# Performance work log

Measured on AMD Instinct MI355X. Metric: run time of the kernel, lower is better.

The kernel has to match this reference:

```python
import jax, jax.numpy as jnp
import numpy as np

TOP_K = 2
EPS = 1e-9

def setup_inputs() -> dict:
    key = jax.random.key(0)
    ks = jax.random.split(key, 8)
    B, L, C, F = 64, 512, 3, 300          # batteries, cycles, channels, curve length
    d_model, d_llm, d_ff, E = 512, 4096, 2048, 8
    s = lambda k, sh: jax.random.normal(k, sh, jnp.float32) * 0.02
    return dict(
        cycle_curve_data=jax.random.normal(ks[0], (B, L, C, F), jnp.float32),
        cycle_numbers=jax.random.uniform(ks[1], (B, 1), jnp.float32),
        DKP_embeddings=jax.random.normal(ks[2], (B, d_llm), jnp.float32),
        gate_W1=s(ks[3], (d_llm + 1, d_ff)), gate_b1=jnp.zeros((d_ff,), jnp.float32),
        gate_W2=s(ks[4], (d_ff, E)), gate_b2=jnp.zeros((E,), jnp.float32),
        expert_W=s(ks[5], (E, C * F, d_model)), expert_b=jnp.zeros((E, d_model), jnp.float32),
        gen_W=s(ks[6], (C * F, d_model)), gen_b=jnp.zeros((d_model,), jnp.float32),
    )

def reference(cycle_curve_data, cycle_numbers, DKP_embeddings,
              gate_W1, gate_b1, gate_W2, gate_b2,
              expert_W, expert_b, gen_W, gen_b):
    B, L, C, F = cycle_curve_data.shape
    # router (PatternRouter_two): 2-layer MLP over [DKP embedding ; cycle number]
    g_in = jnp.concatenate([DKP_embeddings, cycle_numbers], axis=-1)   # [B, d_llm+1]
    h = jax.nn.gelu(g_in @ gate_W1 + gate_b1)
    logits = h @ gate_W2 + gate_b2                                     # [B, E]
    # top-k mask on raw logits (as in source), softmax, mask, renormalize
    _, idx = jax.lax.top_k(logits, TOP_K)
    mask = jnp.zeros(logits.shape, bool).at[jnp.arange(B)[:, None], idx].set(True)
    p = jax.nn.softmax(logits, axis=1)
    g = jnp.where(mask, p, 0.0)
    gates = g / (jnp.sum(g, axis=1, keepdims=True) + EPS)              # [B, E]
    # experts: flatten(start_dim=2) then Linear(3*F -> d_model); combine is linear
    # so fold gates into a per-battery weight: sum_e gates[b,e] * W_e
    x = cycle_curve_data.reshape(B, L, C * F)                          # [B, L, 3F]
    Wb = jnp.einsum('be,eid->bid', gates, expert_W)                    # [B, 3F, d]
    bb = gates @ expert_b                                              # [B, d]
    moe_out = jnp.einsum('bli,bid->bld', x, Wb) + bb[:, None, :]       # [B, L, d]
    general = x @ gen_W + gen_b                                        # [B, L, d]
    # source casts the combined MoE output to bf16 before adding
    return general + moe_out.astype(jnp.bfloat16)
```

## Files before the change

kernel.cpp:

```cpp
#include <hip/hip_runtime.h>
#include <hip/hip_bf16.h>
#include <stdint.h>

typedef __attribute__((ext_vector_type(8))) short short8;
typedef __attribute__((ext_vector_type(4))) short short4v;
typedef __attribute__((ext_vector_type(4))) float f32x4;

__device__ inline unsigned short f2bf(float f) {
    union { float f; uint32_t u; } v; v.f = f;
    uint32_t u = v.u;
    uint32_t r = (u + 0x7FFFu + ((u >> 16) & 1u)) >> 16;
    return (unsigned short)r;
}

__device__ inline short4v pk4(float4 a) {
    short4v r;
    r[0] = (short)f2bf(a.x); r[1] = (short)f2bf(a.y);
    r[2] = (short)f2bf(a.z); r[3] = (short)f2bf(a.w);
    return r;
}

__global__ __launch_bounds__(256) void router1(const float* __restrict__ DKP,
                                               const float* __restrict__ W1,
                                               float* __restrict__ part) {
    __shared__ float gin[16 * 256];
    const int t   = threadIdx.x;
    const int lin = blockIdx.x + 16 * blockIdx.y;
    const int jc  = lin & 7;
    const int bg  = (lin >> 3) & 3;
    const int ks  = lin >> 5;
    const int k0  = ks * 256;
    {
        const int b = t >> 4, q = t & 15;
        #pragma unroll
        for (int s = 0; s < 4; ++s)
            *(float4*)(gin + b * 256 + q * 16 + s * 4) =
                *(const float4*)(DKP + (size_t)(bg * 16 + b) * 4096 + k0 + q * 16 + s * 4);
    }
    __syncthreads();
    const int ja = jc * 256 + t;
    float accA[16];
    #pragma unroll
    for (int b = 0; b < 16; ++b) accA[b] = 0.f;
    float wcur[8], wnxt[8];
    #pragma unroll
    for (int i = 0; i < 8; ++i)
        wcur[i] = W1[(size_t)(k0 + i) * 2048 + ja];
    #pragma unroll 2
    for (int oct = 0; oct < 32; ++oct) {
        const int kk = oct * 8;
        if (oct < 31) {
            #pragma unroll
            for (int i = 0; i < 8; ++i)
                wnxt[i] = W1[(size_t)(k0 + kk + 8 + i) * 2048 + ja];
        }
        #pragma unroll
        for (int b = 0; b < 16; ++b) {
            float4 g0 = *(const float4*)(gin + b * 256 + kk);
            float4 g1 = *(const float4*)(gin + b * 256 + kk + 4);
            accA[b] += g0.x*wcur[0] + g0.y*wcur[1] + g0.z*wcur[2] + g0.w*wcur[3]
                     + g1.x*wcur[4] + g1.y*wcur[5] + g1.z*wcur[6] + g1.w*wcur[7];
        }
        #pragma unroll
        for (int i = 0; i < 8; ++i) wcur[i] = wnxt[i];
    }
    #pragma unroll 1
    for (int b = 0; b < 16; ++b)
        part[((size_t)(ks * 64 + bg * 16 + b)) * 2048 + ja] = accA[b];
}

__global__ __launch_bounds__(256) void router2p(const float* __restrict__ part,
                                                const float* __restrict__ cyc,
                                                const float* __restrict__ W1,
                                                const float* __restrict__ b1,
                                                const float* __restrict__ W2,
                                                float* __restrict__ plog) {
    __shared__ float red[256 * 8];
    const int b = blockIdx.x, jc = blockIdx.y;
    const int t = threadIdx.x;
    const int j = jc * 256 + t;
    float s = 0.f;
    #pragma unroll
    for (int tt = 0; tt < 16; ++tt)
        s += part[((size_t)tt * 64 + b) * 2048 + j];
    s += cyc[b] * W1[(size_t)4096 * 2048 + j] + b1[j];
    const float u  = s + 0.044715f * s * s * s;
    const float th = tanhf(0.7978845608028654f * u);
    const float hv = 0.5f * s * (1.0f + th);
    const float* w = W2 + (size_t)j * 8;
    #pragma unroll
    for (int e = 0; e < 8; ++e) red[t * 8 + e] = hv * w[e];
    __syncthreads();
    if (t < 8) {
        float acc = 0.f;
        for (int r = 0; r < 256; ++r) acc += red[r * 8 + t];
        plog[((size_t)b * 8 + jc) * 8 + t] = acc;
    }
}

__global__ __launch_bounds__(64) void router4(const float* __restrict__ plog,
                                              const float* __restrict__ b2,
                                              float4* __restrict__ gates) {
    const int b = threadIdx.x;
    float l[8];
    #pragma unroll
    for (int e = 0; e < 8; ++e) l[e] = b2[e];
    #pragma unroll
    for (int jc = 0; jc < 8; ++jc)
        #pragma unroll
        for (int e = 0; e < 8; ++e)
            l[e] += plog[((size_t)b * 8 + jc) * 8 + e];
    int e0 = 0;
    #pragma unroll
    for (int e = 1; e < 8; ++e) if (l[e] > l[e0]) e0 = e;
    int e1 = (e0 == 0) ? 1 : 0;
    #pragma unroll
    for (int e = 0; e < 8; ++e) if (e != e0 && l[e] > l[e1]) e1 = e;
    const float m = l[e0];
    float p[8], Z = 0.f;
    #pragma unroll
    for (int e = 0; e < 8; ++e) { p[e] = expf(l[e] - m); Z += p[e]; }
    const float pe0 = p[e0] / Z, pe1 = p[e1] / Z;
    const float s2 = pe0 + pe1 + 1e-9f;
    gates[b] = make_float4(__int_as_float(e0), __int_as_float(e1), pe0 / s2, pe1 / s2);
}

__global__ __launch_bounds__(256) void combine_w(const float* __restrict__ genW,
                                                 const float* __restrict__ expW,
                                                 const float4* __restrict__ gates,
                                                 unsigned short* __restrict__ wc) {
    __shared__ float T[9][32 * 36];
    __shared__ float4 gsh[64];
    const int t  = threadIdx.x;
    const int d0 = blockIdx.x * 32;
    const int i0 = blockIdx.y * 32;
    if (t < 64) gsh[t] = gates[t];
    {
        const int il = t >> 3, d4 = (t & 7) * 4;
        const int i = i0 + il;
        const bool valid = (i < 900);
        const size_t off = (size_t)i * 512 + d0 + d4;
        #pragma unroll
        for (int s = 0; s < 9; ++s) {
            const float* src = (s == 0) ? genW : (expW + (size_t)(s - 1) * 900 * 512);
            float4 v = valid ? *(const float4*)(src + off) : make_float4(0, 0, 0, 0);
            float* Td = &T[s][0];
            Td[(d4 + 0) * 36 + il] = v.x;
            Td[(d4 + 1) * 36 + il] = v.y;
            Td[(d4 + 2) * 36 + il] = v.z;
            Td[(d4 + 3) * 36 + il] = v.w;
        }
    }
    __syncthreads();
    const int bb = t >> 7;
    const int dl = (t >> 2) & 31;
    const int sg = t & 3;
    const int fo = dl * 36 + sg * 8;
    unsigned short* wrow = wc + (size_t)(d0 + dl) * 928 + i0 + sg * 8;
    #pragma unroll 2
    for (int bp = 0; bp < 32; ++bp) {
        const int b = bp * 2 + bb;
        const float4 gt = gsh[b];
        const int e0 = __float_as_int(gt.x), e1 = __float_as_int(gt.y);
        const float g0 = gt.z, g1 = gt.w;
        float4 Ga = *(const float4*)&T[0][fo],      Gb = *(const float4*)&T[0][fo + 4];
        float4 Xa = *(const float4*)&T[1 + e0][fo], Xb = *(const float4*)&T[1 + e0][fo + 4];
        float4 Ya = *(const float4*)&T[1 + e1][fo], Yb = *(const float4*)&T[1 + e1][fo + 4];
        short8 r;
        r[0] = (short)f2bf(Ga.x + g0 * Xa.x + g1 * Ya.x);
        r[1] = (short)f2bf(Ga.y + g0 * Xa.y + g1 * Ya.y);
        r[2] = (short)f2bf(Ga.z + g0 * Xa.z + g1 * Ya.z);
        r[3] = (short)f2bf(Ga.w + g0 * Xa.w + g1 * Ya.w);
        r[4] = (short)f2bf(Gb.x + g0 * Xb.x + g1 * Yb.x);
        r[5] = (short)f2bf(Gb.y + g0 * Xb.y + g1 * Yb.y);
        r[6] = (short)f2bf(Gb.z + g0 * Xb.z + g1 * Yb.z);
        r[7] = (short)f2bf(Gb.w + g0 * Xb.w + g1 * Yb.w);
        *(short8*)(wrow + (size_t)b * 512 * 928) = r;
    }
}

__global__ __launch_bounds__(512) void moe_gemm(const float* __restrict__ x,
                                                const unsigned short* __restrict__ wc,
                                                const float4* __restrict__ gates,
                                                const float* __restrict__ eb,
                                                const float* __restrict__ genb,
                                                float* __restrict__ out) {
    __shared__ unsigned short As[2][64 * 40];
    __shared__ unsigned short Bs[4][512 * 32];
    const int g  = blockIdx.x;
    const int b  = (g & 7) + 8 * (g >> 6);
    const int m0 = ((g >> 3) & 7) * 64;
    const int t = threadIdx.x, lane = t & 63, wid = t >> 6;
    const float4 gt = gates[b];
    const int e0 = __float_as_int(gt.x), e1 = __float_as_int(gt.y);
    const float g0 = gt.z, g1 = gt.w;
    const float* xb = x + (size_t)b * 512 * 900;
    const unsigned short* wcb = wc + (size_t)b * 512 * 928;
    f32x4 acc[4][4];
    #pragma unroll
    for (int mi = 0; mi < 4; ++mi)
        #pragma unroll
        for (int ni = 0; ni < 4; ++ni)
            acc[mi][ni] = (f32x4){0.f, 0.f, 0.f, 0.f};

    const int arow  = t >> 3;
    const int akoff = (t & 7) * 4;
    const float* xrow = xb + (size_t)(m0 + arow) * 900 + akoff;
    const int bseg = (lane & 3) ^ ((lane >> 3) & 3);
    const int burow = lane >> 2;

    const int wn = wid * 64;
    const int lm = lane & 15, lq = lane >> 4;

    auto loadA = [&](int kt) -> float4 {
        if (kt < 28) return *(const float4*)(xrow + kt * 32);
        const float* p = xrow + 896 - (akoff ? 32 : 0);
        float4 raw = *(const float4*)p;
        if (akoff) raw = make_float4(0.f, 0.f, 0.f, 0.f);
        return raw;
    };
    auto stageB = [&](int buf, int kt) {
        const int k0 = kt * 32;
        #pragma unroll
        for (int r = 0; r < 4; ++r) {
            const int chunk = wid * 4 + r;
            const int n = chunk * 16 + burow;
            const unsigned short* gsrc = wcb + (size_t)n * 928 + k0 + bseg * 8;
            unsigned short* ldst = &Bs[buf][chunk * 512];
            __builtin_amdgcn_global_load_lds(
                (const __attribute__((address_space(1))) unsigned int*)gsrc,
                (__attribute__((address_space(3))) unsigned int*)ldst, 16, 0, 0);
        }
    };
    auto packA = [&](int buf, float4 f) {
        *(short4v*)&As[buf][arow * 40 + akoff] = pk4(f);
    };
    auto compute = [&](int buf) {
        short8 af[4], bfr[4];
        #pragma unroll
        for (int mi = 0; mi < 4; ++mi)
            af[mi] = *(const short8*)&As[buf & 1][(mi * 16 + lm) * 40 + lq * 8];
        #pragma unroll
        for (int ni = 0; ni < 4; ++ni) {
            const int n = wn + ni * 16 + lm;
            const int slot = lq ^ ((lm >> 1) & 3);
            bfr[ni] = *(const short8*)&Bs[buf][n * 32 + slot * 8];
        }
        #pragma unroll
        for (int mi = 0; mi < 4; ++mi)
            #pragma unroll
            for (int ni = 0; ni < 4; ++ni)
                acc[mi][ni] = __builtin_amdgcn_mfma_f32_16x16x32_bf16(
                    af[mi], bfr[ni], acc[mi][ni], 0, 0, 0);
    };

#define BARN(n) asm volatile("s_waitcnt vmcnt(" #n ") lgkmcnt(0)\n\ts_barrier" ::: "memory")

    float4 a_next;
    {
        float4 a0 = loadA(0);
        stageB(0, 0);
        a_next = loadA(1);
        stageB(1, 1);
        stageB(2, 2);
        packA(0, a0);
        BARN(9);
    }
    #pragma unroll 1
    for (int q = 0; q < 6; ++q) {
        const int tb = q * 4;
        { float4 a2 = loadA(tb + 2); stageB(3, tb + 3); compute(0); packA(1, a_next); a_next = a2; BARN(9); }
        { float4 a2 = loadA(tb + 3); stageB(0, tb + 4); compute(1); packA(0, a_next); a_next = a2; BARN(9); }
        { float4 a2 = loadA(tb + 4); stageB(1, tb + 5); compute(2); packA(1, a_next); a_next = a2; BARN(9); }
        { float4 a2 = loadA(tb + 5); stageB(2, tb + 6); compute(3); packA(0, a_next); a_next = a2; BARN(9); }
    }
    { float4 a2 = loadA(26); stageB(3, 27); compute(0); packA(1, a_next); a_next = a2; BARN(9); }
    { float4 a2 = loadA(27); stageB(0, 28); compute(1); packA(0, a_next); a_next = a2; BARN(9); }
    { float4 a2 = loadA(28); compute(2); packA(1, a_next); a_next = a2; BARN(5); }
    { compute(3); packA(0, a_next); BARN(0); }
    compute(0);

#undef BARN

    #pragma unroll
    for (int ni = 0; ni < 4; ++ni) {
        const int col = wn + ni * 16 + lm;
        const float bias = genb[col] + g0 * eb[e0 * 512 + col] + g1 * eb[e1 * 512 + col];
        #pragma unroll
        for (int mi = 0; mi < 4; ++mi) {
            const int row = m0 + mi * 16 + lq * 4;
            #pragma unroll
            for (int r = 0; r < 4; ++r)
                out[((size_t)b * 512 + row + r) * 512 + col] = acc[mi][ni][r] + bias;
        }
    }
}

extern "C" void kernel_launch(void* const* d_in, const int* in_sizes, int n_in,
                              void* d_out, int out_size, void* d_ws, size_t ws_size,
                              hipStream_t stream) {
    const float* x    = (const float*)d_in[0];
    const float* cyc  = (const float*)d_in[1];
    const float* dkp  = (const float*)d_in[2];
    const float* gW1  = (const float*)d_in[3];
    const float* gb1  = (const float*)d_in[4];
    const float* gW2  = (const float*)d_in[5];
    const float* gb2  = (const float*)d_in[6];
    const float* eW   = (const float*)d_in[7];
    const float* eb   = (const float*)d_in[8];
    const float* genW = (const float*)d_in[9];
    const float* genb = (const float*)d_in[10];
    float* out = (float*)d_out;

    char* ws = (char*)d_ws;
    unsigned short* wcomb = (unsigned short*)ws;
    float* part  = (float*)ws;
    float4* gts  = (float4*)(ws + 60817408);
    float* plog  = (float*)(ws + 60817408 + 1024);

    router1<<<dim3(16, 32), 256, 0, stream>>>(dkp, gW1, part);
    router2p<<<dim3(64, 8), 256, 0, stream>>>(part, cyc, gW1, gb1, gW2, plog);
    router4<<<1, 64, 0, stream>>>(plog, gb2, gts);
    combine_w<<<dim3(16, 29), 256, 0, stream>>>(genW, eW, gts, wcomb);
    moe_gemm<<<512, 512, 0, stream>>>(x, wcomb, gts, eb, genb, out);
}
```

Measured before the change: 335.2 us.

## Retile router and MoE GEMM, use k-slab weight layout and 128-row tiles

```diff
diff --git a/kernel.cpp b/kernel.cpp
--- a/kernel.cpp
+++ b/kernel.cpp
@@ -13,60 +13,62 @@
     return (unsigned short)r;
 }
 
-__device__ inline short4v pk4(float4 a) {
-    short4v r;
+__device__ inline short8 pk8(float4 a, float4 b) {
+    short8 r;
     r[0] = (short)f2bf(a.x); r[1] = (short)f2bf(a.y);
     r[2] = (short)f2bf(a.z); r[3] = (short)f2bf(a.w);
+    r[4] = (short)f2bf(b.x); r[5] = (short)f2bf(b.y);
+    r[6] = (short)f2bf(b.z); r[7] = (short)f2bf(b.w);
     return r;
 }
 
 __global__ __launch_bounds__(256) void router1(const float* __restrict__ DKP,
                                                const float* __restrict__ W1,
                                                float* __restrict__ part) {
-    __shared__ float gin[16 * 256];
-    const int t   = threadIdx.x;
-    const int lin = blockIdx.x + 16 * blockIdx.y;
-    const int jc  = lin & 7;
-    const int bg  = (lin >> 3) & 3;
-    const int ks  = lin >> 5;
-    const int k0  = ks * 256;
+    __shared__ float gin[16 * 64];
+    const int t  = threadIdx.x;
+    const int g  = blockIdx.x;
+    const int jc = g & 1;
+    const int bg = (g >> 3) & 3;
+    const int ks = ((g >> 1) & 3) | ((g >> 5) << 2);
+    const int k0 = ks * 64;
     {
-        const int b = t >> 4, q = t & 15;
-        #pragma unroll
-        for (int s = 0; s < 4; ++s)
-            *(float4*)(gin + b * 256 + q * 16 + s * 4) =
-                *(const float4*)(DKP + (size_t)(bg * 16 + b) * 4096 + k0 + q * 16 + s * 4);
+        const int bl = t >> 4, q = t & 15;
+        *(float4*)(gin + bl * 64 + q * 4) =
+            *(const float4*)(DKP + (size_t)(bg * 16 + bl) * 4096 + k0 + q * 4);
     }
     __syncthreads();
-    const int ja = jc * 256 + t;
-    float accA[16];
-    #pragma unroll
-    for (int b = 0; b < 16; ++b) accA[b] = 0.f;
-    float wcur[8], wnxt[8];
+    const int ja = jc * 1024 + t * 4;
+    f32x4 acc[16];
+    #pragma unroll
+    for (int bl = 0; bl < 16; ++bl) acc[bl] = (f32x4){0.f, 0.f, 0.f, 0.f};
+    f32x4 wcur[8], wnxt[8];
     #pragma unroll
     for (int i = 0; i < 8; ++i)
-        wcur[i] = W1[(size_t)(k0 + i) * 2048 + ja];
-    #pragma unroll 2
-    for (int oct = 0; oct < 32; ++oct) {
+        wcur[i] = *(const f32x4*)(W1 + (size_t)(k0 + i) * 2048 + ja);
+    #pragma unroll 1
+    for (int oct = 0; oct < 8; ++oct) {
         const int kk = oct * 8;
-        if (oct < 31) {
+        if (oct < 7) {
             #pragma unroll
             for (int i = 0; i < 8; ++i)
-                wnxt[i] = W1[(size_t)(k0 + kk + 8 + i) * 2048 + ja];
-        }
-        #pragma unroll
-        for (int b = 0; b < 16; ++b) {
-            float4 g0 = *(const float4*)(gin + b * 256 + kk);
-            float4 g1 = *(const float4*)(gin + b * 256 + kk + 4);
-            accA[b] += g0.x*wcur[0] + g0.y*wcur[1] + g0.z*wcur[2] + g0.w*wcur[3]
-                     + g1.x*wcur[4] + g1.y*wcur[5] + g1.z*wcur[6] + g1.w*wcur[7];
+                wnxt[i] = *(const f32x4*)(W1 + (size_t)(k0 + kk + 8 + i) * 2048 + ja);
+        }
+        #pragma unroll
+        for (int bl = 0; bl < 16; ++bl) {
+            float4 g0 = *(const float4*)(gin + bl * 64 + kk);
+            float4 g1 = *(const float4*)(gin + bl * 64 + kk + 4);
+            f32x4 a = acc[bl];
+            a = a + wcur[0] * g0.x + wcur[1] * g0.y + wcur[2] * g0.z + wcur[3] * g0.w
+                  + wcur[4] * g1.x + wcur[5] * g1.y + wcur[6] * g1.z + wcur[7] * g1.w;
+            acc[bl] = a;
         }
         #pragma unroll
         for (int i = 0; i < 8; ++i) wcur[i] = wnxt[i];
     }
     #pragma unroll 1
-    for (int b = 0; b < 16; ++b)
-        part[((size_t)(ks * 64 + bg * 16 + b)) * 2048 + ja] = accA[b];
+    for (int bl = 0; bl < 16; ++bl)
+        *(f32x4*)(part + ((size_t)(ks * 64 + bg * 16 + bl)) * 2048 + ja) = acc[bl];
 }
 
 __global__ __launch_bounds__(256) void router2p(const float* __restrict__ part,
@@ -80,8 +82,8 @@
     const int t = threadIdx.x;
     const int j = jc * 256 + t;
     float s = 0.f;
-    #pragma unroll
-    for (int tt = 0; tt < 16; ++tt)
+    #pragma unroll 8
+    for (int tt = 0; tt < 64; ++tt)
         s += part[((size_t)tt * 64 + b) * 2048 + j];
     s += cyc[b] * W1[(size_t)4096 * 2048 + j] + b1[j];
     const float u  = s + 0.044715f * s * s * s;
@@ -133,7 +135,8 @@
     __shared__ float4 gsh[64];
     const int t  = threadIdx.x;
     const int d0 = blockIdx.x * 32;
-    const int i0 = blockIdx.y * 32;
+    const int kt = blockIdx.y;
+    const int i0 = kt * 32;
     if (t < 64) gsh[t] = gates[t];
     {
         const int il = t >> 3, d4 = (t & 7) * 4;
@@ -156,7 +159,7 @@
     const int dl = (t >> 2) & 31;
     const int sg = t & 3;
     const int fo = dl * 36 + sg * 8;
-    unsigned short* wrow = wc + (size_t)(d0 + dl) * 928 + i0 + sg * 8;
+    unsigned short* wrow = wc + (size_t)kt * 16384 + (d0 + dl) * 32 + sg * 8;
     #pragma unroll 2
     for (int bp = 0; bp < 32; ++bp) {
         const int b = bp * 2 + bb;
@@ -175,120 +178,121 @@
         r[5] = (short)f2bf(Gb.y + g0 * Xb.y + g1 * Yb.y);
         r[6] = (short)f2bf(Gb.z + g0 * Xb.z + g1 * Yb.z);
         r[7] = (short)f2bf(Gb.w + g0 * Xb.w + g1 * Yb.w);
-        *(short8*)(wrow + (size_t)b * 512 * 928) = r;
-    }
-}
-
-__global__ __launch_bounds__(512) void moe_gemm(const float* __restrict__ x,
-                                                const unsigned short* __restrict__ wc,
-                                                const float4* __restrict__ gates,
-                                                const float* __restrict__ eb,
-                                                const float* __restrict__ genb,
-                                                float* __restrict__ out) {
-    __shared__ unsigned short As[2][64 * 40];
-    __shared__ unsigned short Bs[4][512 * 32];
+        *(short8*)(wrow + (size_t)b * 475136) = r;
+    }
+}
+
+__global__ __launch_bounds__(512, 1) void moe_gemm(const float* __restrict__ x,
+                                                   const unsigned short* __restrict__ wc,
+                                                   const float4* __restrict__ gates,
+                                                   const float* __restrict__ eb,
+                                                   const float* __restrict__ genb,
+                                                   float* __restrict__ out) {
+    __shared__ unsigned short As[2][128 * 40];
+    __shared__ unsigned short Bs[2][512 * 32];
     const int g  = blockIdx.x;
-    const int b  = (g & 7) + 8 * (g >> 6);
-    const int m0 = ((g >> 3) & 7) * 64;
+    const int b  = (g & 7) + 8 * (g >> 5);
+    const int m0 = ((g >> 3) & 3) * 128;
     const int t = threadIdx.x, lane = t & 63, wid = t >> 6;
     const float4 gt = gates[b];
     const int e0 = __float_as_int(gt.x), e1 = __float_as_int(gt.y);
     const float g0 = gt.z, g1 = gt.w;
     const float* xb = x + (size_t)b * 512 * 900;
-    const unsigned short* wcb = wc + (size_t)b * 512 * 928;
-    f32x4 acc[4][4];
+    const unsigned short* wcb = wc + (size_t)b * 475136;
+    f32x4 acc[4][8];
     #pragma unroll
     for (int mi = 0; mi < 4; ++mi)
         #pragma unroll
-        for (int ni = 0; ni < 4; ++ni)
+        for (int ni = 0; ni < 8; ++ni)
             acc[mi][ni] = (f32x4){0.f, 0.f, 0.f, 0.f};
 
-    const int arow  = t >> 3;
-    const int akoff = (t & 7) * 4;
-    const float* xrow = xb + (size_t)(m0 + arow) * 900 + akoff;
-    const int bseg = (lane & 3) ^ ((lane >> 3) & 3);
+    const int arow = t >> 2;
+    const int acol = (t & 3) * 8;
+    const float* xrow = xb + (size_t)(m0 + arow) * 900 + acol;
+    const int bseg  = (lane & 3) ^ ((lane >> 3) & 3);
     const int burow = lane >> 2;
 
-    const int wn = wid * 64;
+    const int wm = wid >> 2;
+    const int wn = (wid & 3) * 128;
     const int lm = lane & 15, lq = lane >> 4;
 
-    auto loadA = [&](int kt) -> float4 {
-        if (kt < 28) return *(const float4*)(xrow + kt * 32);
-        const float* p = xrow + 896 - (akoff ? 32 : 0);
-        float4 raw = *(const float4*)p;
-        if (akoff) raw = make_float4(0.f, 0.f, 0.f, 0.f);
-        return raw;
-    };
     auto stageB = [&](int buf, int kt) {
-        const int k0 = kt * 32;
+        const unsigned short* slab = wcb + (size_t)kt * 16384;
         #pragma unroll
         for (int r = 0; r < 4; ++r) {
             const int chunk = wid * 4 + r;
-            const int n = chunk * 16 + burow;
-            const unsigned short* gsrc = wcb + (size_t)n * 928 + k0 + bseg * 8;
+            const unsigned short* gsrc = slab + (chunk * 16 + burow) * 32 + bseg * 8;
             unsigned short* ldst = &Bs[buf][chunk * 512];
             __builtin_amdgcn_global_load_lds(
                 (const __attribute__((address_space(1))) unsigned int*)gsrc,
                 (__attribute__((address_space(3))) unsigned int*)ldst, 16, 0, 0);
         }
     };
-    auto packA = [&](int buf, float4 f) {
-        *(short4v*)&As[buf][arow * 40 + akoff] = pk4(f);
+    auto loadA = [&](int kt, float4& lo, float4& hi) {
+        if (kt < 28) {
+            lo = *(const float4*)(xrow + kt * 32);
+            hi = *(const float4*)(xrow + kt * 32 + 4);
+        } else {
+            lo = make_float4(0.f, 0.f, 0.f, 0.f);
+            hi = make_float4(0.f, 0.f, 0.f, 0.f);
+            if (acol == 0) lo = *(const float4*)(xb + (size_t)(m0 + arow) * 900 + 896);
+        }
+    };
+    auto packA = [&](int buf, float4 lo, float4 hi) {
+        *(short8*)&As[buf][arow * 40 + acol] = pk8(lo, hi);
     };
     auto compute = [&](int buf) {
-        short8 af[4], bfr[4];
+        short8 af[4];
         #pragma unroll
         for (int mi = 0; mi < 4; ++mi)
-            af[mi] = *(const short8*)&As[buf & 1][(mi * 16 + lm) * 40 + lq * 8];
-        #pragma unroll
-        for (int ni = 0; ni < 4; ++ni) {
+            af[mi] = *(const short8*)&As[buf][(wm * 64 + mi * 16 + lm) * 40 + lq * 8];
+        #pragma unroll
+        for (int ni = 0; ni < 8; ++ni) {
             const int n = wn + ni * 16 + lm;
             const int slot = lq ^ ((lm >> 1) & 3);
-            bfr[ni] = *(const short8*)&Bs[buf][n * 32 + slot * 8];
-        }
-        #pragma unroll
-        for (int mi = 0; mi < 4; ++mi)
+            short8 bf = *(const short8*)&Bs[buf][n * 32 + slot * 8];
             #pragma unroll
-            for (int ni = 0; ni < 4; ++ni)
+            for (int mi = 0; mi < 4; ++mi)
                 acc[mi][ni] = __builtin_amdgcn_mfma_f32_16x16x32_bf16(
-                    af[mi], bfr[ni], acc[mi][ni], 0, 0, 0);
+                    af[mi], bf, acc[mi][ni], 0, 0, 0);
+        }
     };
 
-#define BARN(n) asm volatile("s_waitcnt vmcnt(" #n ") lgkmcnt(0)\n\ts_barrier" ::: "memory")
-
-    float4 a_next;
     {
-        float4 a0 = loadA(0);
+        float4 lo, hi;
+        loadA(0, lo, hi);
         stageB(0, 0);
-        a_next = loadA(1);
-        stageB(1, 1);
-        stageB(2, 2);
-        packA(0, a0);
-        BARN(9);
+        packA(0, lo, hi);
+        __syncthreads();
     }
     #pragma unroll 1
-    for (int q = 0; q < 6; ++q) {
-        const int tb = q * 4;
-        { float4 a2 = loadA(tb + 2); stageB(3, tb + 3); compute(0); packA(1, a_next); a_next = a2; BARN(9); }
-        { float4 a2 = loadA(tb + 3); stageB(0, tb + 4); compute(1); packA(0, a_next); a_next = a2; BARN(9); }
-        { float4 a2 = loadA(tb + 4); stageB(1, tb + 5); compute(2); packA(1, a_next); a_next = a2; BARN(9); }
-        { float4 a2 = loadA(tb + 5); stageB(2, tb + 6); compute(3); packA(0, a_next); a_next = a2; BARN(9); }
-    }
-    { float4 a2 = loadA(26); stageB(3, 27); compute(0); packA(1, a_next); a_next = a2; BARN(9); }
-    { float4 a2 = loadA(27); stageB(0, 28); compute(1); packA(0, a_next); a_next = a2; BARN(9); }
-    { float4 a2 = loadA(28); compute(2); packA(1, a_next); a_next = a2; BARN(5); }
-    { compute(3); packA(0, a_next); BARN(0); }
+    for (int p = 0; p < 14; ++p) {
+        {
+            float4 lo, hi;
+            loadA(2 * p + 1, lo, hi);
+            stageB(1, 2 * p + 1);
+            compute(0);
+            packA(1, lo, hi);
+            __syncthreads();
+        }
+        {
+            float4 lo, hi;
+            loadA(2 * p + 2, lo, hi);
+            stageB(0, 2 * p + 2);
+            compute(1);
+            packA(0, lo, hi);
+            __syncthreads();
+        }
+    }
     compute(0);
 
-#undef BARN
-
-    #pragma unroll
-    for (int ni = 0; ni < 4; ++ni) {
+    #pragma unroll
+    for (int ni = 0; ni < 8; ++ni) {
         const int col = wn + ni * 16 + lm;
         const float bias = genb[col] + g0 * eb[e0 * 512 + col] + g1 * eb[e1 * 512 + col];
         #pragma unroll
         for (int mi = 0; mi < 4; ++mi) {
-            const int row = m0 + mi * 16 + lq * 4;
+            const int row = m0 + wm * 64 + mi * 16 + lq * 4;
             #pragma unroll
             for (int r = 0; r < 4; ++r)
                 out[((size_t)b * 512 + row + r) * 512 + col] = acc[mi][ni][r] + bias;
@@ -318,9 +322,9 @@
     float4* gts  = (float4*)(ws + 60817408);
     float* plog  = (float*)(ws + 60817408 + 1024);
 
-    router1<<<dim3(16, 32), 256, 0, stream>>>(dkp, gW1, part);
+    router1<<<512, 256, 0, stream>>>(dkp, gW1, part);
     router2p<<<dim3(64, 8), 256, 0, stream>>>(part, cyc, gW1, gb1, gW2, plog);
     router4<<<1, 64, 0, stream>>>(plog, gb2, gts);
     combine_w<<<dim3(16, 29), 256, 0, stream>>>(genW, eW, gts, wcomb);
-    moe_gemm<<<512, 512, 0, stream>>>(x, wcomb, gts, eb, genb, out);
-}
+    moe_gemm<<<256, 512, 0, stream>>>(x, wcomb, gts, eb, genb, out);
+}
```

New measurement: 324.0 us. 3.3% less time.
